# Kernel tuning notes

Measured on AMD Instinct MI355X. Metric: run time of the kernel, lower is better.

The kernel has to match this reference:

```python
import jax, jax.numpy as jnp
import numpy as np

BETA, ALPHA, NS_STEPS = 0.9, 1.0, 1
D_MODEL, D_STATE, D_CONV, EXPAND = 768, 16, 4, 2
D_INNER = EXPAND * D_MODEL
DT_RANK = -(-D_MODEL // 16)  # ceil(d_model/16) = 48
B, L = 2, 1024


def setup_inputs() -> dict:
    key = jax.random.key(0)
    ks = jax.random.split(key, 8)
    s = lambda k, shape, sc=0.02: jax.random.normal(k, shape, jnp.float32) * sc
    return {
        "hidden_states": jax.random.normal(ks[0], (B, L, D_MODEL), jnp.float32),
        "in_proj_w": s(ks[1], (2 * D_INNER, D_MODEL)),
        "conv_w": s(ks[2], (D_INNER, 1, D_CONV), 0.2),
        "conv_b": jnp.zeros((D_INNER,), jnp.float32),
        "x_proj_w": s(ks[3], (DT_RANK + 2 * D_STATE, D_INNER)),
        "dt_head_w": s(ks[4], (D_INNER, DT_RANK)),
        "dt_head_b": s(ks[5], (D_INNER,), 0.1),
        "out_proj_w": s(ks[6], (D_MODEL, D_INNER)),
        "D": jnp.ones((D_INNER,), jnp.float32),
    }


def _newton_schulz(G, steps):
    """Muon-style quintic Newton-Schulz orthogonalization of (b, d, n) with d >= n."""
    a, b, c = 3.4445, -4.7750, 2.0315
    X = G / (jnp.linalg.norm(G, axis=(-2, -1), keepdims=True) + 1e-7)
    X = X.swapaxes(-2, -1)  # (b, n, d): rows <= cols
    for _ in range(steps):
        A = X @ X.swapaxes(-2, -1)       # (b, n, n) small Gram
        Bm = b * A + c * (A @ A)
        X = a * X + Bm @ X
    return X.swapaxes(-2, -1)            # back to (b, d, n)


def reference(hidden_states, in_proj_w, conv_w, conv_b, x_proj_w, dt_head_w, dt_head_b, out_proj_w, D):
    Bz, Lz, _ = hidden_states.shape
    dtype = hidden_states.dtype
    # input projection -> x, z  (B, L, d_inner) each
    xz = jnp.einsum('bld,ed->ble', hidden_states, in_proj_w)
    x, z = jnp.split(xz, 2, axis=-1)
    # causal depthwise conv over time + SiLU
    xc = jax.lax.conv_general_dilated(
        x.swapaxes(1, 2), conv_w, (1,), [(D_CONV - 1, 0)],
        dimension_numbers=('NCH', 'OIH', 'NCH'), feature_group_count=D_INNER)
    x = jax.nn.silu(xc.swapaxes(1, 2) + conv_b)  # (B, L, d_inner)
    # projections for dt / k / q
    x_dbl = jnp.einsum('bld,ed->ble', x, x_proj_w)
    dt_low, k, q = jnp.split(x_dbl, [DT_RANK, DT_RANK + D_STATE], axis=-1)
    dt = jnp.einsum('blr,dr->bld', dt_low, dt_head_w)  # (B, L, d_inner), bias applied in scan

    def step(carry, inp):
        v, h = carry  # velocity / hidden states, each (b, d_inner, d_state)
        x_t, dt_t, k_t, q_t = inp
        dt_t = jax.nn.sigmoid(dt_t + dt_head_b)                              # (b, d)
        dt_t = dt_t / (1.0 + dt_t * jnp.sum(k_t * k_t, axis=-1, keepdims=True))
        dA = 1.0 - dt_t[:, :, None] * (k_t * k_t)[:, None, :]                # (b, d, n)
        G = (dt_t * x_t)[:, :, None] * k_t[:, None, :]                       # dt * u * k
        v = BETA * v + ALPHA * _newton_schulz(G, NS_STEPS)
        h = dA * h + v
        y_t = jnp.einsum('bdn,bn->bd', h, q_t) + D * x_t
        return (v, h), y_t

    init = (jnp.zeros((Bz, D_INNER, D_STATE), dtype),
            jnp.zeros((Bz, D_INNER, D_STATE), dtype))
    xs = (x.swapaxes(0, 1), dt.swapaxes(0, 1), k.swapaxes(0, 1), q.swapaxes(0, 1))
    _, y = jax.lax.scan(step, init, xs)        # (L, B, d_inner)
    y = y.swapaxes(0, 1) * jax.nn.silu(z)      # gate
    return jnp.einsum('bld,od->blo', y, out_proj_w)
```

## Files before the change

kernel.cpp:

```cpp
#include <hip/hip_runtime.h>

#define D_MODEL 768
#define D_STATE 16
#define D_INNER 1536
#define DT_RANK 48
#define NB 2
#define LSEQ 1024
#define NROWS (NB * LSEQ)
#define CCH 8
#define CLEN (LSEQ / CCH)
#define BETA_CL 1.3900845e-06f

typedef __attribute__((ext_vector_type(4))) float f32x4;
typedef __attribute__((ext_vector_type(8))) short s16x8;
typedef __attribute__((ext_vector_type(8))) unsigned short u16x8;

__device__ __forceinline__ unsigned short f2bu(float f) {
  unsigned int x = __builtin_bit_cast(unsigned int, f);
  x += 0x7fffu + ((x >> 16) & 1u);
  return (unsigned short)(x >> 16);
}
__device__ __forceinline__ float bfu(unsigned short u) {
  unsigned int x = ((unsigned int)u) << 16;
  return __builtin_bit_cast(float, x);
}

#define CVT_TOTAL 663552
#define Z1_GROUPS 20480
#define Z2_GROUPS 196608
__global__ __launch_bounds__(256) void cvt5z_kernel(const float* __restrict__ s0,
                                                    const float* __restrict__ s1,
                                                    const float* __restrict__ s2,
                                                    const float* __restrict__ s3,
                                                    const float* __restrict__ s4,
                                                    unsigned short* __restrict__ d0,
                                                    unsigned short* __restrict__ d1,
                                                    unsigned short* __restrict__ d2,
                                                    unsigned short* __restrict__ d3,
                                                    unsigned short* __restrict__ d4,
                                                    float* __restrict__ z1,
                                                    float* __restrict__ z2) {
  int g = blockIdx.x * 256 + threadIdx.x;
  if (g >= CVT_TOTAL) {
    int zg = g - CVT_TOTAL;
    f32x4 zero = {0.f, 0.f, 0.f, 0.f};
    if (zg < Z1_GROUPS) {
      *(f32x4*)(z1 + zg * 8) = zero;
      *(f32x4*)(z1 + zg * 8 + 4) = zero;
    } else if (zg < Z1_GROUPS + Z2_GROUPS) {
      int i = (zg - Z1_GROUPS) * 8;
      *(f32x4*)(z2 + i) = zero;
      *(f32x4*)(z2 + i + 4) = zero;
    }
    return;
  }
  const float* s;
  unsigned short* d;
  int base;
  if (g < 196608)      { s = s0; d = d0; base = 0; }
  else if (g < 491520) { s = s1; d = d1; base = 196608; }
  else if (g < 506880) { s = s2; d = d2; base = 491520; }
  else if (g < 516096) { s = s3; d = d3; base = 506880; }
  else                 { s = s4; d = d4; base = 516096; }
  int i = (g - base) * 8;
  f32x4 a = *(const f32x4*)(s + i);
  f32x4 b = *(const f32x4*)(s + i + 4);
  u16x8 o;
#pragma unroll
  for (int j = 0; j < 4; j++) { o[j] = f2bu(a[j]); o[4 + j] = f2bu(b[j]); }
  *(u16x8*)(d + i) = o;
}

template <bool ATOMIC>
__global__ __launch_bounds__(256) void gemm128(const unsigned short* __restrict__ A,
                                               const unsigned short* __restrict__ B,
                                               float* __restrict__ C, int K,
                                               int lda, int ldb, int ldc, int kseg_len) {
  __shared__ __align__(16) unsigned short As[2][128][40];
  __shared__ __align__(16) unsigned short Bs[2][128][40];
  const int m0 = blockIdx.y * 128, n0 = blockIdx.x * 128;
  const int kbeg = blockIdx.z * kseg_len;
  const int kend = kbeg + kseg_len;
  const int t = threadIdx.x;
  const int wave = t >> 6, lane = t & 63;
  const int wm = wave >> 1, wn = wave & 1;
  const int quad = lane >> 4, l16 = lane & 15;
  const int arow = t >> 1, kh = (t & 1) * 16;
  const unsigned short* Ap = A + (size_t)(m0 + arow) * lda + kh;
  const unsigned short* Bp = B + (size_t)(n0 + arow) * ldb + kh;

  u16x8 ra0, ra1, rb0, rb1;
  auto pref = [&](int k0) {
    ra0 = *(const u16x8*)(Ap + k0);
    ra1 = *(const u16x8*)(Ap + k0 + 8);
    rb0 = *(const u16x8*)(Bp + k0);
    rb1 = *(const u16x8*)(Bp + k0 + 8);
  };
  auto tolds = [&](int bi) {
    *(u16x8*)&As[bi][arow][kh] = ra0;
    *(u16x8*)&As[bi][arow][kh + 8] = ra1;
    *(u16x8*)&Bs[bi][arow][kh] = rb0;
    *(u16x8*)&Bs[bi][arow][kh + 8] = rb1;
  };

  f32x4 acc[4][4] = {};
  pref(kbeg);
  tolds(0);
  __syncthreads();
  int buf = 0;
  for (int k0 = kbeg; k0 < kend; k0 += 32) {
    const bool more = (k0 + 32 < kend);
    if (more) pref(k0 + 32);
    s16x8 af[4], bf[4];
#pragma unroll
    for (int i = 0; i < 4; i++) {
      af[i] = *(const s16x8*)&As[buf][wm * 64 + i * 16 + l16][quad * 8];
      bf[i] = *(const s16x8*)&Bs[buf][wn * 64 + i * 16 + l16][quad * 8];
    }
#pragma unroll
    for (int mi = 0; mi < 4; mi++)
#pragma unroll
      for (int ni = 0; ni < 4; ni++)
        acc[mi][ni] = __builtin_amdgcn_mfma_f32_16x16x32_bf16(af[mi], bf[ni], acc[mi][ni], 0, 0, 0);
    if (more) tolds(buf ^ 1);
    __syncthreads();
    buf ^= 1;
  }
#pragma unroll
  for (int mi = 0; mi < 4; mi++)
#pragma unroll
    for (int ni = 0; ni < 4; ni++)
#pragma unroll
      for (int r = 0; r < 4; r++) {
        int row = m0 + wm * 64 + mi * 16 + quad * 4 + r;
        int col = n0 + wn * 64 + ni * 16 + l16;
        if constexpr (ATOMIC)
          atomicAdd(&C[(size_t)row * ldc + col], acc[mi][ni][r]);
        else
          C[(size_t)row * ldc + col] = acc[mi][ni][r];
      }
}

template <bool ATOMIC>
__global__ __launch_bounds__(256) void gemm_bt(const unsigned short* __restrict__ Ab,
                                               const unsigned short* __restrict__ B,
                                               float* __restrict__ C, int M, int N, int K,
                                               int lda, int ldb, int ldc, int kseg_len) {
  __shared__ __align__(16) unsigned short As[2][64][40];
  __shared__ __align__(16) unsigned short Bs[2][64][40];
  const int m0 = blockIdx.y * 64, n0 = blockIdx.x * 64;
  const int kbeg = blockIdx.z * kseg_len;
  const int kend = (kbeg + kseg_len < K) ? (kbeg + kseg_len) : K;
  const int t = threadIdx.x;
  const int wave = t >> 6, lane = t & 63;
  const int wm = wave >> 1, wn = wave & 1;
  const int quad = lane >> 4, l16 = lane & 15;
  const int srow = t >> 2;
  const int kseg = (t & 3) * 8;
  const bool va = (m0 + srow) < M, vb = (n0 + srow) < N;
  const unsigned short* Bp = B + (size_t)(n0 + srow) * ldb;

  u16x8 rab, rbb;
  auto pref = [&](int k0) {
    const int kk = k0 + kseg;
    const int krem = kend - kk;
    const unsigned short* Ap = Ab + (size_t)(m0 + srow) * lda + kk;
    if (va && krem >= 8) {
      rab = *(const u16x8*)Ap;
    } else {
#pragma unroll
      for (int j = 0; j < 8; j++) rab[j] = (va && j < krem) ? Ap[j] : (unsigned short)0;
    }
    if (vb && krem >= 8) {
      rbb = *(const u16x8*)(Bp + kk);
    } else {
#pragma unroll
      for (int j = 0; j < 8; j++) rbb[j] = (vb && j < krem) ? Bp[kk + j] : (unsigned short)0;
    }
  };
  auto tolds = [&](int bi) {
    *(u16x8*)&As[bi][srow][kseg] = rab;
    *(u16x8*)&Bs[bi][srow][kseg] = rbb;
  };

  f32x4 acc[2][2] = {};
  pref(kbeg);
  tolds(0);
  __syncthreads();
  int buf = 0;
  for (int k0 = kbeg; k0 < kend; k0 += 32) {
    const bool more = (k0 + 32 < kend);
    if (more) pref(k0 + 32);
    s16x8 a0 = *(const s16x8*)&As[buf][wm * 32 + l16][quad * 8];
    s16x8 a1 = *(const s16x8*)&As[buf][wm * 32 + 16 + l16][quad * 8];
    s16x8 b0 = *(const s16x8*)&Bs[buf][wn * 32 + l16][quad * 8];
    s16x8 b1 = *(const s16x8*)&Bs[buf][wn * 32 + 16 + l16][quad * 8];
    acc[0][0] = __builtin_amdgcn_mfma_f32_16x16x32_bf16(a0, b0, acc[0][0], 0, 0, 0);
    acc[0][1] = __builtin_amdgcn_mfma_f32_16x16x32_bf16(a0, b1, acc[0][1], 0, 0, 0);
    acc[1][0] = __builtin_amdgcn_mfma_f32_16x16x32_bf16(a1, b0, acc[1][0], 0, 0, 0);
    acc[1][1] = __builtin_amdgcn_mfma_f32_16x16x32_bf16(a1, b1, acc[1][1], 0, 0, 0);
    if (more) tolds(buf ^ 1);
    __syncthreads();
    buf ^= 1;
  }
#pragma unroll
  for (int mi = 0; mi < 2; mi++)
#pragma unroll
    for (int ni = 0; ni < 2; ni++)
#pragma unroll
      for (int r = 0; r < 4; r++) {
        int row = m0 + wm * 32 + mi * 16 + quad * 4 + r;
        int col = n0 + wn * 32 + ni * 16 + l16;
        if (row < M && col < N) {
          if constexpr (ATOMIC)
            atomicAdd(&C[(size_t)row * ldc + col], acc[mi][ni][r]);
          else
            C[(size_t)row * ldc + col] = acc[mi][ni][r];
        }
      }
}

__global__ __launch_bounds__(256) void conv_silu_kernel(const float* __restrict__ xz,
                                                        const float* __restrict__ cw,
                                                        const float* __restrict__ cb,
                                                        const float* __restrict__ Dp,
                                                        float* __restrict__ xc,
                                                        unsigned short* __restrict__ xcb,
                                                        float* __restrict__ szb,
                                                        unsigned short* __restrict__ gzb) {
  int idx = blockIdx.x * 256 + threadIdx.x;
  if (idx >= NROWS * D_INNER) return;
  int c = idx % D_INNER;
  int row = idx / D_INNER;
  int b = row >> 10;
  int l = row & (LSEQ - 1);
  float acc = cb[c];
#pragma unroll
  for (int j = 0; j < 4; j++) {
    int dl = l - 3 + j;
    if (dl >= 0) acc += xz[(size_t)(row - 3 + j) * 3072 + c] * cw[c * 4 + j];
  }
  float sg = 1.0f / (1.0f + expf(-acc));
  float val = acc * sg;
  xc[idx] = val;
  xcb[idx] = f2bu(val);
  float z = xz[(size_t)row * 3072 + 1536 + c];
  float sz = z / (1.0f + expf(-z));
  size_t bo = (((size_t)(b * 96 + (c >> 4))) * LSEQ + l) * 16 + (c & 15);
  szb[bo] = sz;
  gzb[bo] = f2bu(Dp[c] * val * sz);
}

__global__ __launch_bounds__(256) void precompute_kernel(const float* __restrict__ xdbl,
                                                         const unsigned short* __restrict__ wdt,
                                                         const float* __restrict__ xconv,
                                                         const float* __restrict__ dtb,
                                                         float* __restrict__ dtblk,
                                                         float* __restrict__ ublk,
                                                         float* __restrict__ kqbuf) {
  int row = blockIdx.x;
  int t = threadIdx.x;
  int b = row >> 10;
  int l = row & (LSEQ - 1);
  __shared__ float xr_s[80];
  if (t < 80) xr_s[t] = xdbl[(size_t)row * 80 + t];
  __syncthreads();
  float nk = 0.0f;
#pragma unroll
  for (int n = 0; n < 16; n++) { float kv = xr_s[48 + n]; nk += kv * kv; }
  float dtf[6], u0[6];
  float nupart = 0.0f;
#pragma unroll
  for (int i = 0; i < 6; i++) {
    int d = i * 256 + t;
    float draw = dtb[d];
    const unsigned short* w = wdt + (size_t)d * 48;
#pragma unroll
    for (int j = 0; j < 6; j++) {
      u16x8 wv = *(const u16x8*)(w + j * 8);
#pragma unroll
      for (int e = 0; e < 8; e++) draw = fmaf(bfu(wv[e]), xr_s[j * 8 + e], draw);
    }
    float sg = 1.0f / (1.0f + expf(-draw));
    float dv = sg / (1.0f + sg * nk);
    dtf[i] = dv;
    float u = dv * xconv[(size_t)row * D_INNER + d];
    u0[i] = u;
    nupart += u * u;
  }
  __shared__ float red[4];
  float v = nupart;
#pragma unroll
  for (int off = 32; off > 0; off >>= 1) v += __shfl_xor(v, off);
  if ((t & 63) == 0) red[t >> 6] = v;
  __syncthreads();
  float nu = red[0] + red[1] + red[2] + red[3];
  float p = nu * nk;
  float s = sqrtf(p) + 1e-7f;
  float tt = p / (s * s);
  float gamma = (3.4445f + tt * (-4.7750f + 2.0315f * tt)) / s;
#pragma unroll
  for (int i = 0; i < 6; i++) {
    int d = i * 256 + t;
    size_t bo = (((size_t)(b * 96 + (d >> 4))) * LSEQ + l) * 16 + (d & 15);
    dtblk[bo] = dtf[i];
    ublk[bo] = gamma * u0[i];
  }
  if (t < 16) {
    kqbuf[(size_t)row * 32 + t] = xr_s[48 + t];
    kqbuf[(size_t)row * 32 + 16 + t] = xr_s[64 + t];
  }
}

__global__ __launch_bounds__(64) void scan_phase1(const float* __restrict__ ublk,
                                                  const float* __restrict__ dtblk,
                                                  const float* __restrict__ kqbuf,
                                                  float* __restrict__ cvp,
                                                  float* __restrict__ chp,
                                                  float* __restrict__ gp,
                                                  float* __restrict__ rp) {
  __shared__ float u_s[2][512];
  __shared__ float dt_s[2][512];
  __shared__ __align__(16) float kq_s[2][32][32];
  const int t = threadIdx.x;
  const int nq = t & 3, dloc = t >> 2;
  const int b = blockIdx.x / (96 * CCH);
  const int rem = blockIdx.x % (96 * CCH);
  const int db = rem / CCH;
  const int c = rem % CCH;
  const int tbase = c * CLEN;
  const float* ubp = ublk + (((size_t)(b * 96 + db)) * LSEQ + tbase) * 16;
  const float* dtp = dtblk + (((size_t)(b * 96 + db)) * LSEQ + tbase) * 16;
  const float* kqb = kqbuf + (size_t)b * LSEQ * 32;
  const int krow0 = t >> 3, kcol = (t & 7) * 4;
  f32x4 pu0, pu1, pd0, pd1, pk[4];
  auto prefetch = [&](int lt) {
    pu0 = *(const f32x4*)(ubp + lt * 16 + t * 8);
    pu1 = *(const f32x4*)(ubp + lt * 16 + t * 8 + 4);
    pd0 = *(const f32x4*)(dtp + lt * 16 + t * 8);
    pd1 = *(const f32x4*)(dtp + lt * 16 + t * 8 + 4);
#pragma unroll
    for (int i = 0; i < 4; i++)
      pk[i] = *(const f32x4*)(kqb + (size_t)(tbase + lt + krow0 + 8 * i) * 32 + kcol);
  };
  auto writelds = [&](int bi) {
    *(f32x4*)&u_s[bi][t * 8] = pu0;
    *(f32x4*)&u_s[bi][t * 8 + 4] = pu1;
    *(f32x4*)&dt_s[bi][t * 8] = pd0;
    *(f32x4*)&dt_s[bi][t * 8 + 4] = pd1;
#pragma unroll
    for (int i = 0; i < 4; i++)
      *(f32x4*)&kq_s[bi][krow0 + 8 * i][kcol] = pk[i];
  };
  f32x4 v = {0.f, 0.f, 0.f, 0.f}, h = {0.f, 0.f, 0.f, 0.f};
  f32x4 g = {0.f, 0.f, 0.f, 0.f}, r = {1.f, 1.f, 1.f, 1.f};
  float bt = 0.9f;
  prefetch(0);
  writelds(0);
  int buf = 0;
  for (int t0 = 0; t0 < CLEN; t0 += 32) {
    const bool more = (t0 + 32 < CLEN);
    if (more) prefetch(t0 + 32);
#pragma unroll 4
    for (int s = 0; s < 32; s++) {
      float u = u_s[buf][s * 16 + dloc];
      float dtf = dt_s[buf][s * 16 + dloc];
      f32x4 kv = *(const f32x4*)&kq_s[buf][s][nq * 4];
#pragma unroll
      for (int j = 0; j < 4; j++) {
        float kj = kv[j];
        v[j] = fmaf(0.9f, v[j], u * kj);
        float a = fmaf(-dtf * kj, kj, 1.0f);
        h[j] = fmaf(a, h[j], v[j]);
        r[j] *= a;
        g[j] = fmaf(a, g[j], bt);
      }
      bt *= 0.9f;
    }
    if (more) writelds(buf ^ 1);
    buf ^= 1;
  }
  size_t o = (((size_t)b * CCH + c) * D_INNER + db * 16 + dloc) * 16 + nq * 4;
  *(f32x4*)(cvp + o) = v;
  *(f32x4*)(chp + o) = h;
  *(f32x4*)(gp + o) = g;
  *(f32x4*)(rp + o) = r;
}

__global__ __launch_bounds__(256) void scan_phase2(const float* __restrict__ cvp,
                                                   const float* __restrict__ chp,
                                                   float* __restrict__ gp,
                                                   float* __restrict__ rp) {
  int i = blockIdx.x * 256 + threadIdx.x;
  int b = i / (D_INNER * 16);
  int rem = i % (D_INNER * 16);
  float v0 = 0.f, h0 = 0.f;
#pragma unroll
  for (int c = 0; c < CCH; c++) {
    size_t o = ((size_t)(b * CCH + c)) * (D_INNER * 16) + rem;
    float cv = cvp[o], ch = chp[o], gg = gp[o], rr = rp[o];
    gp[o] = v0;
    rp[o] = h0;
    float v0n = fmaf(BETA_CL, v0, cv);
    float h0n = fmaf(gg, v0, fmaf(rr, h0, ch));
    v0 = v0n;
    h0 = h0n;
  }
}

__global__ __launch_bounds__(64) void scan_phase3(const float* __restrict__ ublk,
                                                  const float* __restrict__ dtblk,
                                                  const float* __restrict__ kqbuf,
                                                  const float* __restrict__ gp,
                                                  const float* __restrict__ rp,
                                                  const float* __restrict__ szb,
                                                  const unsigned short* __restrict__ gzb,
                                                  unsigned short* __restrict__ ygb) {
  __shared__ float u_s[2][512];
  __shared__ float dt_s[2][512];
  __shared__ float sz_s[2][512];
  __shared__ unsigned short gz_s[2][512];
  __shared__ __align__(16) float kq_s[2][32][32];
  const int t = threadIdx.x;
  const int nq = t & 3, dloc = t >> 2;
  const int b = blockIdx.x / (96 * CCH);
  const int rem = blockIdx.x % (96 * CCH);
  const int db = rem / CCH;
  const int c = rem % CCH;
  const int tbase = c * CLEN;
  const size_t blkoff = (((size_t)(b * 96 + db)) * LSEQ + tbase) * 16;
  const float* ubp = ublk + blkoff;
  const float* dtp = dtblk + blkoff;
  const float* szp = szb + blkoff;
  const unsigned short* gzp = gzb + blkoff;
  const float* kqb = kqbuf + (size_t)b * LSEQ * 32;
  unsigned short* y_p = ygb + (size_t)b * LSEQ * D_INNER + db * 16 + dloc;
  const int krow0 = t >> 3, kcol = (t & 7) * 4;
  f32x4 pu0, pu1, pd0, pd1, ps0, ps1, pk[4];
  u16x8 pg;
  auto prefetch = [&](int lt) {
    pu0 = *(const f32x4*)(ubp + lt * 16 + t * 8);
    pu1 = *(const f32x4*)(ubp + lt * 16 + t * 8 + 4);
    pd0 = *(const f32x4*)(dtp + lt * 16 + t * 8);
    pd1 = *(const f32x4*)(dtp + lt * 16 + t * 8 + 4);
    ps0 = *(const f32x4*)(szp + lt * 16 + t * 8);
    ps1 = *(const f32x4*)(szp + lt * 16 + t * 8 + 4);
    pg = *(const u16x8*)(gzp + lt * 16 + t * 8);
#pragma unroll
    for (int i = 0; i < 4; i++)
      pk[i] = *(const f32x4*)(kqb + (size_t)(tbase + lt + krow0 + 8 * i) * 32 + kcol);
  };
  auto writelds = [&](int bi) {
    *(f32x4*)&u_s[bi][t * 8] = pu0;
    *(f32x4*)&u_s[bi][t * 8 + 4] = pu1;
    *(f32x4*)&dt_s[bi][t * 8] = pd0;
    *(f32x4*)&dt_s[bi][t * 8 + 4] = pd1;
    *(f32x4*)&sz_s[bi][t * 8] = ps0;
    *(f32x4*)&sz_s[bi][t * 8 + 4] = ps1;
    *(u16x8*)&gz_s[bi][t * 8] = pg;
#pragma unroll
    for (int i = 0; i < 4; i++)
      *(f32x4*)&kq_s[bi][krow0 + 8 * i][kcol] = pk[i];
  };
  size_t so = (((size_t)b * CCH + c) * D_INNER + db * 16 + dloc) * 16 + nq * 4;
  f32x4 v = *(const f32x4*)(gp + so);
  f32x4 h = *(const f32x4*)(rp + so);
  prefetch(0);
  writelds(0);
  int buf = 0;
  for (int t0 = 0; t0 < CLEN; t0 += 32) {
    const bool more = (t0 + 32 < CLEN);
    if (more) prefetch(t0 + 32);
#pragma unroll 4
    for (int s = 0; s < 32; s++) {
      float u = u_s[buf][s * 16 + dloc];
      float dtf = dt_s[buf][s * 16 + dloc];
      f32x4 kv = *(const f32x4*)&kq_s[buf][s][nq * 4];
      f32x4 qv = *(const f32x4*)&kq_s[buf][s][16 + nq * 4];
      float yp = 0.0f;
#pragma unroll
      for (int j = 0; j < 4; j++) {
        float kj = kv[j];
        v[j] = fmaf(0.9f, v[j], u * kj);
        float dA = fmaf(-dtf * kj, kj, 1.0f);
        h[j] = fmaf(dA, h[j], v[j]);
        yp = fmaf(h[j], qv[j], yp);
      }
      yp += __shfl_xor(yp, 1);
      yp += __shfl_xor(yp, 2);
      if (nq == 0) {
        float val = fmaf(yp, sz_s[buf][s * 16 + dloc], bfu(gz_s[buf][s * 16 + dloc]));
        y_p[(size_t)(tbase + t0 + s) * D_INNER] = f2bu(val);
      }
    }
    if (more) writelds(buf ^ 1);
    buf ^= 1;
  }
}

extern "C" void kernel_launch(void* const* d_in, const int* in_sizes, int n_in,
                              void* d_out, int out_size, void* d_ws, size_t ws_size,
                              hipStream_t stream) {
  const float* hidden = (const float*)d_in[0];
  const float* w_in   = (const float*)d_in[1];
  const float* conv_w = (const float*)d_in[2];
  const float* conv_b = (const float*)d_in[3];
  const float* w_x    = (const float*)d_in[4];
  const float* w_dt   = (const float*)d_in[5];
  const float* b_dt   = (const float*)d_in[6];
  const float* w_out  = (const float*)d_in[7];
  const float* Dp     = (const float*)d_in[8];

  float* ws    = (float*)d_ws;
  float* xz    = ws;
  float* xconv = xz + (size_t)NROWS * 3072;
  float* xdbl  = xconv + (size_t)NROWS * D_INNER;
  float* dtblk = xdbl + (size_t)NROWS * 80;
  float* ublk  = dtblk + (size_t)NROWS * D_INNER;
  float* kqbuf = ublk + (size_t)NROWS * D_INNER;
  float* szblk = kqbuf + (size_t)NROWS * 32;
  const size_t PL = (size_t)NB * CCH * D_INNER * 16;
  float* cvp   = szblk + (size_t)NROWS * D_INNER;
  float* chp   = cvp + PL;
  float* gp    = chp + PL;
  float* rp    = gp + PL;
  unsigned short* bfr = (unsigned short*)(rp + PL);
  unsigned short* hbf = bfr;
  unsigned short* wib = hbf + 1572864;
  unsigned short* wxb = wib + 2359296;
  unsigned short* wdb = wxb + 122880;
  unsigned short* wob = wdb + 73728;
  unsigned short* xcb = wob + 1179648;
  unsigned short* ygb = xcb + 3145728;
  unsigned short* gzblk = hbf;

  dim3 blk(256);
  cvt5z_kernel<<<dim3((CVT_TOTAL + Z1_GROUPS + Z2_GROUPS) / 256), blk, 0, stream>>>(
      hidden, w_in, w_x, w_dt, w_out, hbf, wib, wxb, wdb, wob, xdbl, (float*)d_out);
  gemm128<false><<<dim3(24, 16, 1), blk, 0, stream>>>(hbf, wib, xz, 768, 768, 768, 3072, 768);
  conv_silu_kernel<<<dim3(12288), blk, 0, stream>>>(xz, conv_w, conv_b, Dp,
                                                    xconv, xcb, szblk, gzblk);
  gemm_bt<true><<<dim3(2, 32, 8), blk, 0, stream>>>(xcb, wxb, xdbl, 2048, 80, 1536,
                                                    1536, 1536, 80, 192);
  precompute_kernel<<<dim3(NROWS), blk, 0, stream>>>(xdbl, wdb, xconv, b_dt, dtblk, ublk, kqbuf);
  scan_phase1<<<dim3(NB * 96 * CCH), dim3(64), 0, stream>>>(ublk, dtblk, kqbuf, cvp, chp, gp, rp);
  scan_phase2<<<dim3(192), blk, 0, stream>>>(cvp, chp, gp, rp);
  scan_phase3<<<dim3(NB * 96 * CCH), dim3(64), 0, stream>>>(ublk, dtblk, kqbuf, gp, rp,
                                                            szblk, gzblk, ygb);
  gemm128<true><<<dim3(6, 16, 4), blk, 0, stream>>>(ygb, wob, (float*)d_out, 384,
                                                    1536, 1536, 768, 384);
}
```

Before: 241.0 us.

## Double scan chunks, fold chunk-carry combine into phase3, emit in_proj output as bf16

Doubles the number of time chunks in the chunked scan so phase1 and phase3 launch twice as many blocks, each with half the sequential length. The separate phase2 carry-propagation kernel is removed, and each phase3 block instead recombines all preceding chunk summaries itself. The input-projection GEMM now writes bf16 instead of fp32, halving the xz write and read traffic in the conv kernel. The trade-offs are redundant, serial carry work that grows with chunk index, and extra rounding error on x and z.

```diff
diff --git a/kernel.cpp b/kernel.cpp
--- a/kernel.cpp
+++ b/kernel.cpp
@@ -7,9 +7,9 @@
 #define NB 2
 #define LSEQ 1024
 #define NROWS (NB * LSEQ)
-#define CCH 8
+#define CCH 16
 #define CLEN (LSEQ / CCH)
-#define BETA_CL 1.3900845e-06f
+#define BETA_CL 1.1790184e-03f
 
 typedef __attribute__((ext_vector_type(4))) float f32x4;
 typedef __attribute__((ext_vector_type(8))) short s16x8;
@@ -71,10 +71,10 @@
   *(u16x8*)(d + i) = o;
 }
 
-template <bool ATOMIC>
+template <bool ATOMIC, bool OUTBF16>
 __global__ __launch_bounds__(256) void gemm128(const unsigned short* __restrict__ A,
                                                const unsigned short* __restrict__ B,
-                                               float* __restrict__ C, int K,
+                                               void* __restrict__ Cv, int K,
                                                int lda, int ldb, int ldc, int kseg_len) {
   __shared__ __align__(16) unsigned short As[2][128][40];
   __shared__ __align__(16) unsigned short Bs[2][128][40];
@@ -134,10 +134,12 @@
       for (int r = 0; r < 4; r++) {
         int row = m0 + wm * 64 + mi * 16 + quad * 4 + r;
         int col = n0 + wn * 64 + ni * 16 + l16;
-        if constexpr (ATOMIC)
-          atomicAdd(&C[(size_t)row * ldc + col], acc[mi][ni][r]);
+        if constexpr (OUTBF16)
+          ((unsigned short*)Cv)[(size_t)row * ldc + col] = f2bu(acc[mi][ni][r]);
+        else if constexpr (ATOMIC)
+          atomicAdd(&((float*)Cv)[(size_t)row * ldc + col], acc[mi][ni][r]);
         else
-          C[(size_t)row * ldc + col] = acc[mi][ni][r];
+          ((float*)Cv)[(size_t)row * ldc + col] = acc[mi][ni][r];
       }
 }
 
@@ -220,7 +222,7 @@
       }
 }
 
-__global__ __launch_bounds__(256) void conv_silu_kernel(const float* __restrict__ xz,
+__global__ __launch_bounds__(256) void conv_silu_kernel(const unsigned short* __restrict__ xzb,
                                                         const float* __restrict__ cw,
                                                         const float* __restrict__ cb,
                                                         const float* __restrict__ Dp,
@@ -238,13 +240,13 @@
 #pragma unroll
   for (int j = 0; j < 4; j++) {
     int dl = l - 3 + j;
-    if (dl >= 0) acc += xz[(size_t)(row - 3 + j) * 3072 + c] * cw[c * 4 + j];
+    if (dl >= 0) acc += bfu(xzb[(size_t)(row - 3 + j) * 3072 + c]) * cw[c * 4 + j];
   }
   float sg = 1.0f / (1.0f + expf(-acc));
   float val = acc * sg;
   xc[idx] = val;
   xcb[idx] = f2bu(val);
-  float z = xz[(size_t)row * 3072 + 1536 + c];
+  float z = bfu(xzb[(size_t)row * 3072 + 1536 + c]);
   float sz = z / (1.0f + expf(-z));
   size_t bo = (((size_t)(b * 96 + (c >> 4))) * LSEQ + l) * 16 + (c & 15);
   szb[bo] = sz;
@@ -387,30 +389,11 @@
   *(f32x4*)(rp + o) = r;
 }
 
-__global__ __launch_bounds__(256) void scan_phase2(const float* __restrict__ cvp,
-                                                   const float* __restrict__ chp,
-                                                   float* __restrict__ gp,
-                                                   float* __restrict__ rp) {
-  int i = blockIdx.x * 256 + threadIdx.x;
-  int b = i / (D_INNER * 16);
-  int rem = i % (D_INNER * 16);
-  float v0 = 0.f, h0 = 0.f;
-#pragma unroll
-  for (int c = 0; c < CCH; c++) {
-    size_t o = ((size_t)(b * CCH + c)) * (D_INNER * 16) + rem;
-    float cv = cvp[o], ch = chp[o], gg = gp[o], rr = rp[o];
-    gp[o] = v0;
-    rp[o] = h0;
-    float v0n = fmaf(BETA_CL, v0, cv);
-    float h0n = fmaf(gg, v0, fmaf(rr, h0, ch));
-    v0 = v0n;
-    h0 = h0n;
-  }
-}
-
 __global__ __launch_bounds__(64) void scan_phase3(const float* __restrict__ ublk,
                                                   const float* __restrict__ dtblk,
                                                   const float* __restrict__ kqbuf,
+                                                  const float* __restrict__ cvp,
+                                                  const float* __restrict__ chp,
                                                   const float* __restrict__ gp,
                                                   const float* __restrict__ rp,
                                                   const float* __restrict__ szb,
@@ -462,10 +445,22 @@
     for (int i = 0; i < 4; i++)
       *(f32x4*)&kq_s[bi][krow0 + 8 * i][kcol] = pk[i];
   };
-  size_t so = (((size_t)b * CCH + c) * D_INNER + db * 16 + dloc) * 16 + nq * 4;
-  f32x4 v = *(const f32x4*)(gp + so);
-  f32x4 h = *(const f32x4*)(rp + so);
   prefetch(0);
+  f32x4 v = {0.f, 0.f, 0.f, 0.f}, h = {0.f, 0.f, 0.f, 0.f};
+  const size_t co = ((size_t)b * CCH * D_INNER + db * 16 + dloc) * 16 + nq * 4;
+  for (int cc = 0; cc < c; cc++) {
+    size_t o = co + (size_t)cc * D_INNER * 16;
+    f32x4 cv = *(const f32x4*)(cvp + o);
+    f32x4 ch = *(const f32x4*)(chp + o);
+    f32x4 gg = *(const f32x4*)(gp + o);
+    f32x4 rr = *(const f32x4*)(rp + o);
+#pragma unroll
+    for (int j = 0; j < 4; j++) {
+      float hn = fmaf(gg[j], v[j], fmaf(rr[j], h[j], ch[j]));
+      v[j] = fmaf(BETA_CL, v[j], cv[j]);
+      h[j] = hn;
+    }
+  }
   writelds(0);
   int buf = 0;
   for (int t0 = 0; t0 < CLEN; t0 += 32) {
@@ -512,8 +507,8 @@
   const float* Dp     = (const float*)d_in[8];
 
   float* ws    = (float*)d_ws;
-  float* xz    = ws;
-  float* xconv = xz + (size_t)NROWS * 3072;
+  unsigned short* xzb = (unsigned short*)ws;
+  float* xconv = ws + (size_t)NROWS * 3072;
   float* xdbl  = xconv + (size_t)NROWS * D_INNER;
   float* dtblk = xdbl + (size_t)NROWS * 80;
   float* ublk  = dtblk + (size_t)NROWS * D_INNER;
@@ -537,16 +532,16 @@
   dim3 blk(256);
   cvt5z_kernel<<<dim3((CVT_TOTAL + Z1_GROUPS + Z2_GROUPS) / 256), blk, 0, stream>>>(
       hidden, w_in, w_x, w_dt, w_out, hbf, wib, wxb, wdb, wob, xdbl, (float*)d_out);
-  gemm128<false><<<dim3(24, 16, 1), blk, 0, stream>>>(hbf, wib, xz, 768, 768, 768, 3072, 768);
-  conv_silu_kernel<<<dim3(12288), blk, 0, stream>>>(xz, conv_w, conv_b, Dp,
+  gemm128<false, true><<<dim3(24, 16, 1), blk, 0, stream>>>(hbf, wib, xzb, 768,
+                                                            768, 768, 3072, 768);
+  conv_silu_kernel<<<dim3(12288), blk, 0, stream>>>(xzb, conv_w, conv_b, Dp,
                                                     xconv, xcb, szblk, gzblk);
   gemm_bt<true><<<dim3(2, 32, 8), blk, 0, stream>>>(xcb, wxb, xdbl, 2048, 80, 1536,
                                                     1536, 1536, 80, 192);
   precompute_kernel<<<dim3(NROWS), blk, 0, stream>>>(xdbl, wdb, xconv, b_dt, dtblk, ublk, kqbuf);
   scan_phase1<<<dim3(NB * 96 * CCH), dim3(64), 0, stream>>>(ublk, dtblk, kqbuf, cvp, chp, gp, rp);
-  scan_phase2<<<dim3(192), blk, 0, stream>>>(cvp, chp, gp, rp);
-  scan_phase3<<<dim3(NB * 96 * CCH), dim3(64), 0, stream>>>(ublk, dtblk, kqbuf, gp, rp,
+  scan_phase3<<<dim3(NB * 96 * CCH), dim3(64), 0, stream>>>(ublk, dtblk, kqbuf, cvp, chp, gp, rp,
                                                             szblk, gzblk, ygb);
-  gemm128<true><<<dim3(6, 16, 4), blk, 0, stream>>>(ygb, wob, (float*)d_out, 384,
-                                                    1536, 1536, 768, 384);
-}
+  gemm128<true, false><<<dim3(6, 16, 4), blk, 0, stream>>>(ygb, wob, (float*)d_out, 384,
+                                                           1536, 1536, 768, 384);
+}
```

Measured after the change: 249.2 us. +3.4%, slower.
